# Kernel tuning notes

Hardware: AMD Instinct MI355X
Metric: run time of the kernel (lower is better)

## Reference

```python
import jax, jax.numpy as jnp
import numpy as np

N = 100000   # nodes
E = 1600000  # edges
HID = 128    # hidden_dim
H = 8        # heads
C = HID // H # head_dim = out_channels per head


def setup_inputs() -> dict:
    key = jax.random.key(0)
    ks = jax.random.split(key, 10)
    x = jax.random.normal(ks[0], (N, HID), jnp.float32)
    edge_index = jax.random.randint(ks[1], (2, E), 0, N, dtype=jnp.int64)
    edge_attr = jax.random.uniform(ks[2], (E,), jnp.float32)
    # GATConv params (lin_src == lin_dst shared since in_channels is int)
    W = jax.random.normal(ks[3], (HID, H * C), jnp.float32) / np.sqrt(HID)
    att_src = jax.random.normal(ks[4], (H, C), jnp.float32) / np.sqrt(C)
    att_dst = jax.random.normal(ks[5], (H, C), jnp.float32) / np.sqrt(C)
    # lin_edge: Linear(edge_dim=1, H*C, bias=False) -> weight [H*C, 1] stored as [H, C]
    w_edge = jax.random.normal(ks[6], (H, C), jnp.float32)
    att_edge = jax.random.normal(ks[7], (H, C), jnp.float32) / np.sqrt(C)
    bias = jnp.zeros((H * C,), jnp.float32)
    gamma = jnp.ones((HID,), jnp.float32)
    beta = jnp.zeros((HID,), jnp.float32)
    return dict(x=x, edge_index=edge_index, edge_attr=edge_attr, W=W,
                att_src=att_src, att_dst=att_dst, w_edge=w_edge,
                att_edge=att_edge, bias=bias, gamma=gamma, beta=beta)


def reference(x, edge_index, edge_attr, W, att_src, att_dst, w_edge, att_edge, bias, gamma, beta):
    n = x.shape[0]
    src, dst = edge_index[0], edge_index[1]
    # add_self_loops with fill_value='mean': loop edge_attr = per-dst-node mean of edge_attr
    ones = jnp.ones_like(edge_attr)
    deg = jax.ops.segment_sum(ones, dst, num_segments=n)
    loop_attr = jax.ops.segment_sum(edge_attr, dst, num_segments=n) / jnp.maximum(deg, 1.0)
    ar = jnp.arange(n, dtype=src.dtype)
    src = jnp.concatenate([src, ar])
    dst = jnp.concatenate([dst, ar])
    ea = jnp.concatenate([edge_attr, loop_attr])  # [E+N]

    h = (x @ W).reshape(n, H, C)                  # [N,H,C]
    a_src = (h * att_src).sum(-1)                 # [N,H]
    a_dst = (h * att_dst).sum(-1)                 # [N,H]
    # edge_dim=1: alpha_edge = <lin_edge(ea), att_edge> = ea * sum(w_edge*att_edge)
    w_e = (w_edge * att_edge).sum(-1)             # [H]
    alpha = a_src[src] + a_dst[dst] + ea[:, None] * w_e  # [E+N, H]
    alpha = jax.nn.leaky_relu(alpha, 0.2)
    # segment softmax over incoming edges of each dst node (all nodes have a self-loop)
    m = jax.ops.segment_max(alpha, dst, num_segments=n)      # [N,H]
    ex = jnp.exp(alpha - m[dst])
    denom = jax.ops.segment_sum(ex, dst, num_segments=n)     # [N,H]
    p = ex / (denom[dst] + 1e-16)
    # scatter-aggregate weighted messages, concat heads, bias
    out = jax.ops.segment_sum(p[:, :, None] * h[src], dst, num_segments=n)
    out = out.reshape(n, H * C) + bias
    # residual + LayerNorm + ReLU
    y = out + x
    mu = y.mean(-1, keepdims=True)
    var = ((y - mu) ** 2).mean(-1, keepdims=True)
    y = (y - mu) * jax.lax.rsqrt(var + 1e-5) * gamma + beta
    return jax.nn.relu(y)
```

## Files before the change

kernel.cpp:

```cpp
#include <hip/hip_runtime.h>
#include <math.h>

#define HID 128
#define HEADS 8
#define CDIM 16
#define NB1 256

typedef short bf8 __attribute__((ext_vector_type(8)));
typedef float f32x4 __attribute__((ext_vector_type(4)));

__device__ __forceinline__ unsigned short f2bf(float f) {
    unsigned u = __float_as_uint(f);
    unsigned r = (u + 0x7fffu + ((u >> 16) & 1u)) >> 16;
    return (unsigned short)r;
}
__device__ __forceinline__ float bf2f(unsigned short u) {
    return __uint_as_float(((unsigned)u) << 16);
}

__global__ __launch_bounds__(256) void k_tw(const float* __restrict__ W,
                                            unsigned short* __restrict__ Wt) {
    int idx = blockIdx.x * 256 + threadIdx.x;
    int j = idx >> 7, k = idx & 127;
    Wt[idx] = f2bf(W[k * HID + j]);
}

__global__ __launch_bounds__(256) void k_hist(const int* __restrict__ dst,
                                              int* __restrict__ cntmat,
                                              int E, int per, int nbkt) {
    __shared__ int h[256];
    int t = threadIdx.x;
    h[t] = 0;
    __syncthreads();
    int b0 = blockIdx.x * per;
    int b1 = min(b0 + per, E);
    for (int e = b0 + t; e < b1; e += 256)
        atomicAdd(&h[dst[e] >> 9], 1);
    __syncthreads();
    if (t < nbkt) cntmat[t * NB1 + blockIdx.x] = h[t];
}

__global__ __launch_bounds__(256) void kscanA(const int* __restrict__ in,
                                              int* __restrict__ tmp,
                                              int* __restrict__ bsum, int M) {
    __shared__ int lds[256];
    int t = threadIdx.x;
    int base = blockIdx.x * 1024 + t * 4;
    int v[4];
#pragma unroll
    for (int i = 0; i < 4; i++) {
        int idx = base + i;
        v[i] = (idx < M) ? in[idx] : 0;
    }
    int s = v[0] + v[1] + v[2] + v[3];
    lds[t] = s;
    __syncthreads();
    for (int off = 1; off < 256; off <<= 1) {
        int xv = (t >= off) ? lds[t - off] : 0;
        __syncthreads();
        lds[t] += xv;
        __syncthreads();
    }
    int run = (t > 0) ? lds[t - 1] : 0;
#pragma unroll
    for (int i = 0; i < 4; i++) {
        int idx = base + i;
        if (idx < M) tmp[idx] = run;
        run += v[i];
    }
    if (t == 255) bsum[blockIdx.x] = lds[255];
}

__global__ __launch_bounds__(128) void kscanB(const int* __restrict__ bsum,
                                              int* __restrict__ bscan, int nb,
                                              const float* __restrict__ w_edge,
                                              const float* __restrict__ att_edge,
                                              float* __restrict__ w_e) {
    __shared__ int lds[128];
    int t = threadIdx.x;
    if (t < HEADS) {
        float s = 0.f;
        for (int c = 0; c < CDIM; c++) s += w_edge[t * CDIM + c] * att_edge[t * CDIM + c];
        w_e[t] = s;
    }
    lds[t] = (t < nb) ? bsum[t] : 0;
    __syncthreads();
    for (int off = 1; off < 128; off <<= 1) {
        int xv = (t >= off) ? lds[t - off] : 0;
        __syncthreads();
        lds[t] += xv;
        __syncthreads();
    }
    bscan[t] = (t > 0) ? lds[t - 1] : 0;
}

__global__ __launch_bounds__(256) void kscanC(const int* __restrict__ tmp,
                                              const int* __restrict__ bscan,
                                              int* __restrict__ ofs, int M) {
    int i = blockIdx.x * 256 + threadIdx.x;
    if (i < M) ofs[i] = tmp[i] + bscan[i >> 10];
}

__global__ __launch_bounds__(256) void k_scat(const int* __restrict__ src,
                                              const int* __restrict__ dst,
                                              const float* __restrict__ eattr,
                                              const int* __restrict__ ofs,
                                              int* __restrict__ d1,
                                              int2* __restrict__ erec1,
                                              int E, int per, int nbkt) {
    __shared__ int cur[256];
    int t = threadIdx.x;
    if (t < nbkt) cur[t] = ofs[t * NB1 + blockIdx.x];
    __syncthreads();
    int b0 = blockIdx.x * per;
    int b1 = min(b0 + per, E);
    for (int e = b0 + t; e < b1; e += 256) {
        int d = dst[e];
        int pos = atomicAdd(&cur[d >> 9], 1);
        d1[pos] = d;
        erec1[pos] = make_int2(src[e], __float_as_int(eattr[e]));
    }
}

__global__ __launch_bounds__(256) void k_bin(const int* __restrict__ ofs,
                                             const int* __restrict__ d1,
                                             const int2* __restrict__ erec1,
                                             int* __restrict__ row_ptr,
                                             int2* __restrict__ erec,
                                             int N, int E, int nbkt) {
    __shared__ int h2[512];
    __shared__ int s2[256];
    __shared__ int cur2[512];
    int b = blockIdx.x, t = threadIdx.x;
    int base = ofs[b * NB1];
    int end = (b + 1 < nbkt) ? ofs[(b + 1) * NB1] : E;
    h2[t] = 0; h2[t + 256] = 0;
    __syncthreads();
    for (int e = base + t; e < end; e += 256)
        atomicAdd(&h2[d1[e] & 511], 1);
    __syncthreads();
    int a0 = h2[2 * t], a1 = h2[2 * t + 1];
    s2[t] = a0 + a1;
    __syncthreads();
    for (int off = 1; off < 256; off <<= 1) {
        int v = (t >= off) ? s2[t - off] : 0;
        __syncthreads();
        s2[t] += v;
        __syncthreads();
    }
    int ex = (t > 0) ? s2[t - 1] : 0;
    int p0 = base + ex;
    int p1 = p0 + a0;
    int ng = b * 512 + 2 * t;
    if (ng <= N) row_ptr[ng] = p0;
    if (ng + 1 <= N) row_ptr[ng + 1] = p1;
    cur2[2 * t] = p0;
    cur2[2 * t + 1] = p1;
    __syncthreads();
    for (int e = base + t; e < end; e += 256) {
        int d = d1[e];
        int pos = atomicAdd(&cur2[d & 511], 1);
        erec[pos] = erec1[e];
    }
}

__global__ __launch_bounds__(256) void k_gemm(const float* __restrict__ x,
                                              const unsigned short* __restrict__ Wt,
                                              const float* __restrict__ att_src,
                                              const float* __restrict__ att_dst,
                                              unsigned short* __restrict__ hbf,
                                              float* __restrict__ a_src,
                                              float* __restrict__ a_dst, int N) {
    int tid = threadIdx.x;
    int wv = tid >> 6, lane = tid & 63;
    int nloc = lane & 15, q = lane >> 4;
    int node = blockIdx.x * 64 + wv * 16 + nloc;
    int nc = min(node, N - 1);
    const float* xp = x + (size_t)nc * HID + q * 8;
    const unsigned short* wp = Wt + nloc * HID + q * 8;
    f32x4 acc[8];
#pragma unroll
    for (int i = 0; i < 8; i++) acc[i] = (f32x4){0.f, 0.f, 0.f, 0.f};
#pragma unroll
    for (int ch = 0; ch < 4; ch++) {
        float4 xv0 = *(const float4*)(xp + ch * 32);
        float4 xv1 = *(const float4*)(xp + ch * 32 + 4);
        bf8 bfrag;
        bfrag[0] = (short)f2bf(xv0.x); bfrag[1] = (short)f2bf(xv0.y);
        bfrag[2] = (short)f2bf(xv0.z); bfrag[3] = (short)f2bf(xv0.w);
        bfrag[4] = (short)f2bf(xv1.x); bfrag[5] = (short)f2bf(xv1.y);
        bfrag[6] = (short)f2bf(xv1.z); bfrag[7] = (short)f2bf(xv1.w);
#pragma unroll
        for (int jt = 0; jt < 8; jt++) {
            bf8 afrag = *(const bf8*)(wp + (size_t)jt * 16 * HID + ch * 32);
            acc[jt] = __builtin_amdgcn_mfma_f32_16x16x32_bf16(afrag, bfrag, acc[jt], 0, 0, 0);
        }
    }
    bool ok = node < N;
    size_t hb = (size_t)nc * HID;
#pragma unroll
    for (int jt = 0; jt < 8; jt++) {
        int j0 = jt * 16 + q * 4;
        float4 as4 = *(const float4*)(att_src + j0);
        float4 ad4 = *(const float4*)(att_dst + j0);
        f32x4 a = acc[jt];
        float ps = a[0] * as4.x + a[1] * as4.y + a[2] * as4.z + a[3] * as4.w;
        float pd = a[0] * ad4.x + a[1] * ad4.y + a[2] * ad4.z + a[3] * ad4.w;
        ps += __shfl_xor(ps, 16, 64); ps += __shfl_xor(ps, 32, 64);
        pd += __shfl_xor(pd, 16, 64); pd += __shfl_xor(pd, 32, 64);
        if (ok) {
            ushort4 hv;
            hv.x = f2bf(a[0]); hv.y = f2bf(a[1]); hv.z = f2bf(a[2]); hv.w = f2bf(a[3]);
            *(ushort4*)(hbf + hb + j0) = hv;
            if (q == 0) {
                a_src[(size_t)node * 8 + jt] = ps;
                a_dst[(size_t)node * 8 + jt] = pd;
            }
        }
    }
}

__global__ __launch_bounds__(64) void k_node(const int* __restrict__ row_ptr,
                                             const int2* __restrict__ erec,
                                             const float* __restrict__ a_src,
                                             const float* __restrict__ a_dst,
                                             const float* __restrict__ w_e,
                                             const unsigned short* __restrict__ hbf,
                                             const float* __restrict__ x,
                                             const float* __restrict__ bias,
                                             const float* __restrict__ gamma,
                                             const float* __restrict__ beta,
                                             float* __restrict__ out, int N) {
    int n = blockIdx.x;
    int lane = threadIdx.x;
    int r0 = row_ptr[n], r1 = row_ptr[n + 1];
    __shared__ float lex[64][9];
    __shared__ int lsrc[64];
    float ad[8], we[8];
#pragma unroll
    for (int q = 0; q < 8; q++) {
        ad[q] = a_dst[(size_t)n * 8 + q];
        we[q] = w_e[q];
    }
    float dsum[8];
#pragma unroll
    for (int q = 0; q < 8; q++) dsum[q] = 0.f;
    float acc0 = 0.f, acc1 = 0.f;
    float suma = 0.f;
    int head = lane >> 3;

    for (int base = r0; base < r1; base += 64) {
        int e = base + lane;
        if (e < r1) {
            int2 rec = erec[e];
            int s = rec.x;
            float a = __int_as_float(rec.y);
            suma += a;
            lsrc[lane] = s;
            const float* asp = a_src + (size_t)s * 8;
#pragma unroll
            for (int q = 0; q < 8; q++) {
                float v = asp[q] + ad[q] + a * we[q];
                v = v > 0.f ? v : 0.2f * v;
                float ex = __expf(v);
                dsum[q] += ex;
                lex[lane][q] = ex;
            }
        }
        __syncthreads();
        int cntc = min(64, r1 - base);
        for (int kk = 0; kk < cntc; kk++) {
            int s = lsrc[kk];
            ushort2 hv = *(const ushort2*)(hbf + (size_t)s * HID + 2 * lane);
            float w = lex[kk][head];
            acc0 = fmaf(w, bf2f(hv.x), acc0);
            acc1 = fmaf(w, bf2f(hv.y), acc1);
        }
        __syncthreads();
    }
#pragma unroll
    for (int q = 0; q < 8; q++) {
        float v = dsum[q];
#pragma unroll
        for (int off = 32; off; off >>= 1) v += __shfl_xor(v, off, 64);
        dsum[q] = v;
    }
#pragma unroll
    for (int off = 32; off; off >>= 1) suma += __shfl_xor(suma, off, 64);

    int deg = r1 - r0;
    float la = suma / fmaxf((float)deg, 1.0f);
    float vs = a_src[(size_t)n * 8 + head] + ad[head] + la * we[head];
    vs = vs > 0.f ? vs : 0.2f * vs;
    float exs = __expf(vs);
    size_t bx = (size_t)n * HID;
    ushort2 hs = *(const ushort2*)(hbf + bx + 2 * lane);
    acc0 = fmaf(exs, bf2f(hs.x), acc0);
    acc1 = fmaf(exs, bf2f(hs.y), acc1);
    float inv = 1.f / (dsum[head] + exs + 1e-16f);

    float2 xv = *(const float2*)(x + bx + 2 * lane);
    float2 bv = *(const float2*)(bias + 2 * lane);
    float y0 = acc0 * inv + bv.x + xv.x;
    float y1 = acc1 * inv + bv.y + xv.y;
    float ss = y0 + y1, sq = y0 * y0 + y1 * y1;
#pragma unroll
    for (int off = 32; off; off >>= 1) {
        ss += __shfl_xor(ss, off, 64);
        sq += __shfl_xor(sq, off, 64);
    }
    float mu = ss * (1.f / 128.f);
    float var = sq * (1.f / 128.f) - mu * mu;
    float r = rsqrtf(fmaxf(var, 0.f) + 1e-5f);
    float2 gv = *(const float2*)(gamma + 2 * lane);
    float2 tv = *(const float2*)(beta + 2 * lane);
    float o0 = (y0 - mu) * r * gv.x + tv.x;
    float o1 = (y1 - mu) * r * gv.y + tv.y;
    float2 ov = make_float2(fmaxf(o0, 0.f), fmaxf(o1, 0.f));
    *(float2*)(out + bx + 2 * lane) = ov;
}

extern "C" void kernel_launch(void* const* d_in, const int* in_sizes, int n_in,
                              void* d_out, int out_size, void* d_ws, size_t ws_size,
                              hipStream_t stream) {
    const float* x        = (const float*)d_in[0];
    const int*   ei       = (const int*)d_in[1];
    const float* eattr    = (const float*)d_in[2];
    const float* W        = (const float*)d_in[3];
    const float* att_src  = (const float*)d_in[4];
    const float* att_dst  = (const float*)d_in[5];
    const float* w_edge   = (const float*)d_in[6];
    const float* att_edge = (const float*)d_in[7];
    const float* bias     = (const float*)d_in[8];
    const float* gamma    = (const float*)d_in[9];
    const float* beta     = (const float*)d_in[10];

    int N = in_sizes[0] / HID;
    int E = in_sizes[2];
    const int* src = ei;
    const int* dst = ei + E;
    float* out = (float*)d_out;

    int nbkt = (N + 511) >> 9;
    int M = nbkt * NB1;
    int per = (E + NB1 - 1) / NB1;

    char* ws = (char*)d_ws;
    size_t off = 0;
    auto alloc = [&](size_t bytes) { char* p = ws + off; off += (bytes + 255) & ~255ull; return p; };
    unsigned short* hbf = (unsigned short*)alloc((size_t)N * HID * 2);
    unsigned short* Wt  = (unsigned short*)alloc((size_t)HID * HID * 2);
    float* a_src   = (float*)alloc((size_t)N * 8 * 4);
    float* a_dst   = (float*)alloc((size_t)N * 8 * 4);
    int2*  erec    = (int2*) alloc((size_t)E * 8);
    int2*  erec1   = (int2*) alloc((size_t)E * 8);
    int*   d1      = (int*)  alloc((size_t)E * 4);
    int*   cntmat  = (int*)  alloc((size_t)M * 4);
    int*   stmp    = (int*)  alloc((size_t)M * 4);
    int*   ofs     = (int*)  alloc((size_t)M * 4);
    int*   bsum    = (int*)  alloc(128 * 4);
    int*   bscan   = (int*)  alloc(128 * 4);
    int*   row_ptr = (int*)  alloc((size_t)(N + 1) * 4);
    float* w_e     = (float*)alloc(8 * 4);

    int nbA = (M + 1023) / 1024;

    k_tw<<<64, 256, 0, stream>>>(W, Wt);
    k_hist<<<NB1, 256, 0, stream>>>(dst, cntmat, E, per, nbkt);
    kscanA<<<nbA, 256, 0, stream>>>(cntmat, stmp, bsum, M);
    kscanB<<<1, 128, 0, stream>>>(bsum, bscan, nbA, w_edge, att_edge, w_e);
    kscanC<<<(M + 255) / 256, 256, 0, stream>>>(stmp, bscan, ofs, M);
    k_scat<<<NB1, 256, 0, stream>>>(src, dst, eattr, ofs, d1, erec1, E, per, nbkt);
    k_bin<<<nbkt, 256, 0, stream>>>(ofs, d1, erec1, row_ptr, erec, N, E, nbkt);
    k_gemm<<<(N + 63) / 64, 256, 0, stream>>>(x, Wt, att_src, att_dst, hbf, a_src, a_dst, N);
    k_node<<<N, 64, 0, stream>>>(row_ptr, erec, a_src, a_dst, w_e, hbf, x,
                                 bias, gamma, beta, out, N);
}
```

Baseline: 338.5 us.

## Co-launch independent kernels and streamline per-node gather in aggregation

Merges the weight transpose into the histogram kernel and the node GEMM into the edge scatter kernel by splitting the grid on block index, so independent work shares one launch and can run concurrently. This removes two launches and lets the GEMM overlap the memory-bound scatter. In the node kernel, the softmax denominator is now accumulated per lane during the gather loop, which removes the 8-way cross-lane reduction. The row offset is made wave-uniform via readfirstlane, a_src is loaded as float4, and bf16 unpacking uses bit masks. The grid-split kernels may reduce occupancy if register or LDS use rises.

```diff
diff --git a/kernel.cpp b/kernel.cpp
--- a/kernel.cpp
+++ b/kernel.cpp
@@ -18,18 +18,19 @@
     return __uint_as_float(((unsigned)u) << 16);
 }
 
-__global__ __launch_bounds__(256) void k_tw(const float* __restrict__ W,
-                                            unsigned short* __restrict__ Wt) {
-    int idx = blockIdx.x * 256 + threadIdx.x;
-    int j = idx >> 7, k = idx & 127;
-    Wt[idx] = f2bf(W[k * HID + j]);
-}
-
-__global__ __launch_bounds__(256) void k_hist(const int* __restrict__ dst,
-                                              int* __restrict__ cntmat,
-                                              int E, int per, int nbkt) {
+__global__ __launch_bounds__(256) void k_hist_tw(const float* __restrict__ W,
+                                                 unsigned short* __restrict__ Wt,
+                                                 const int* __restrict__ dst,
+                                                 int* __restrict__ cntmat,
+                                                 int E, int per, int nbkt) {
     __shared__ int h[256];
     int t = threadIdx.x;
+    if (blockIdx.x >= NB1) {
+        int idx = (blockIdx.x - NB1) * 256 + t;
+        int j = idx >> 7, k = idx & 127;
+        Wt[idx] = f2bf(W[k * HID + j]);
+        return;
+    }
     h[t] = 0;
     __syncthreads();
     int b0 = blockIdx.x * per;
@@ -101,80 +102,34 @@
     if (i < M) ofs[i] = tmp[i] + bscan[i >> 10];
 }
 
-__global__ __launch_bounds__(256) void k_scat(const int* __restrict__ src,
-                                              const int* __restrict__ dst,
-                                              const float* __restrict__ eattr,
-                                              const int* __restrict__ ofs,
-                                              int* __restrict__ d1,
-                                              int2* __restrict__ erec1,
-                                              int E, int per, int nbkt) {
+__global__ __launch_bounds__(256) void k_scat_gemm(
+        const int* __restrict__ src, const int* __restrict__ dst,
+        const float* __restrict__ eattr, const int* __restrict__ ofs,
+        int* __restrict__ d1, int2* __restrict__ erec1,
+        int E, int per, int nbkt,
+        const float* __restrict__ x, const unsigned short* __restrict__ Wt,
+        const float* __restrict__ att_src, const float* __restrict__ att_dst,
+        unsigned short* __restrict__ hbf, float* __restrict__ a_src,
+        float* __restrict__ a_dst, int N) {
     __shared__ int cur[256];
-    int t = threadIdx.x;
-    if (t < nbkt) cur[t] = ofs[t * NB1 + blockIdx.x];
-    __syncthreads();
-    int b0 = blockIdx.x * per;
-    int b1 = min(b0 + per, E);
-    for (int e = b0 + t; e < b1; e += 256) {
-        int d = dst[e];
-        int pos = atomicAdd(&cur[d >> 9], 1);
-        d1[pos] = d;
-        erec1[pos] = make_int2(src[e], __float_as_int(eattr[e]));
-    }
-}
-
-__global__ __launch_bounds__(256) void k_bin(const int* __restrict__ ofs,
-                                             const int* __restrict__ d1,
-                                             const int2* __restrict__ erec1,
-                                             int* __restrict__ row_ptr,
-                                             int2* __restrict__ erec,
-                                             int N, int E, int nbkt) {
-    __shared__ int h2[512];
-    __shared__ int s2[256];
-    __shared__ int cur2[512];
-    int b = blockIdx.x, t = threadIdx.x;
-    int base = ofs[b * NB1];
-    int end = (b + 1 < nbkt) ? ofs[(b + 1) * NB1] : E;
-    h2[t] = 0; h2[t + 256] = 0;
-    __syncthreads();
-    for (int e = base + t; e < end; e += 256)
-        atomicAdd(&h2[d1[e] & 511], 1);
-    __syncthreads();
-    int a0 = h2[2 * t], a1 = h2[2 * t + 1];
-    s2[t] = a0 + a1;
-    __syncthreads();
-    for (int off = 1; off < 256; off <<= 1) {
-        int v = (t >= off) ? s2[t - off] : 0;
-        __syncthreads();
-        s2[t] += v;
-        __syncthreads();
-    }
-    int ex = (t > 0) ? s2[t - 1] : 0;
-    int p0 = base + ex;
-    int p1 = p0 + a0;
-    int ng = b * 512 + 2 * t;
-    if (ng <= N) row_ptr[ng] = p0;
-    if (ng + 1 <= N) row_ptr[ng + 1] = p1;
-    cur2[2 * t] = p0;
-    cur2[2 * t + 1] = p1;
-    __syncthreads();
-    for (int e = base + t; e < end; e += 256) {
-        int d = d1[e];
-        int pos = atomicAdd(&cur2[d & 511], 1);
-        erec[pos] = erec1[e];
-    }
-}
-
-__global__ __launch_bounds__(256) void k_gemm(const float* __restrict__ x,
-                                              const unsigned short* __restrict__ Wt,
-                                              const float* __restrict__ att_src,
-                                              const float* __restrict__ att_dst,
-                                              unsigned short* __restrict__ hbf,
-                                              float* __restrict__ a_src,
-                                              float* __restrict__ a_dst, int N) {
     int tid = threadIdx.x;
+    if (blockIdx.x < NB1) {
+        if (tid < nbkt) cur[tid] = ofs[tid * NB1 + blockIdx.x];
+        __syncthreads();
+        int b0 = blockIdx.x * per;
+        int b1 = min(b0 + per, E);
+        for (int e = b0 + tid; e < b1; e += 256) {
+            int d = dst[e];
+            int pos = atomicAdd(&cur[d >> 9], 1);
+            d1[pos] = d;
+            erec1[pos] = make_int2(src[e], __float_as_int(eattr[e]));
+        }
+        return;
+    }
+    int bid = blockIdx.x - NB1;
     int wv = tid >> 6, lane = tid & 63;
     int nloc = lane & 15, q = lane >> 4;
-    int node = blockIdx.x * 64 + wv * 16 + nloc;
+    int node = bid * 64 + wv * 16 + nloc;
     int nc = min(node, N - 1);
     const float* xp = x + (size_t)nc * HID + q * 8;
     const unsigned short* wp = Wt + nloc * HID + q * 8;
@@ -220,6 +175,48 @@
     }
 }
 
+__global__ __launch_bounds__(256) void k_bin(const int* __restrict__ ofs,
+                                             const int* __restrict__ d1,
+                                             const int2* __restrict__ erec1,
+                                             int* __restrict__ row_ptr,
+                                             int2* __restrict__ erec,
+                                             int N, int E, int nbkt) {
+    __shared__ int h2[512];
+    __shared__ int s2[256];
+    __shared__ int cur2[512];
+    int b = blockIdx.x, t = threadIdx.x;
+    int base = ofs[b * NB1];
+    int end = (b + 1 < nbkt) ? ofs[(b + 1) * NB1] : E;
+    h2[t] = 0; h2[t + 256] = 0;
+    __syncthreads();
+    for (int e = base + t; e < end; e += 256)
+        atomicAdd(&h2[d1[e] & 511], 1);
+    __syncthreads();
+    int a0 = h2[2 * t], a1 = h2[2 * t + 1];
+    s2[t] = a0 + a1;
+    __syncthreads();
+    for (int off = 1; off < 256; off <<= 1) {
+        int v = (t >= off) ? s2[t - off] : 0;
+        __syncthreads();
+        s2[t] += v;
+        __syncthreads();
+    }
+    int ex = (t > 0) ? s2[t - 1] : 0;
+    int p0 = base + ex;
+    int p1 = p0 + a0;
+    int ng = b * 512 + 2 * t;
+    if (ng <= N) row_ptr[ng] = p0;
+    if (ng + 1 <= N) row_ptr[ng + 1] = p1;
+    cur2[2 * t] = p0;
+    cur2[2 * t + 1] = p1;
+    __syncthreads();
+    for (int e = base + t; e < end; e += 256) {
+        int d = d1[e];
+        int pos = atomicAdd(&cur2[d & 511], 1);
+        erec[pos] = erec1[e];
+    }
+}
+
 __global__ __launch_bounds__(64) void k_node(const int* __restrict__ row_ptr,
                                              const int2* __restrict__ erec,
                                              const float* __restrict__ a_src,
@@ -242,10 +239,8 @@
         ad[q] = a_dst[(size_t)n * 8 + q];
         we[q] = w_e[q];
     }
-    float dsum[8];
-#pragma unroll
-    for (int q = 0; q < 8; q++) dsum[q] = 0.f;
     float acc0 = 0.f, acc1 = 0.f;
+    float wsum = 0.f;
     float suma = 0.f;
     int head = lane >> 3;
 
@@ -256,34 +251,29 @@
             int s = rec.x;
             float a = __int_as_float(rec.y);
             suma += a;
-            lsrc[lane] = s;
-            const float* asp = a_src + (size_t)s * 8;
+            lsrc[lane] = s << 8;
+            const float4* asp = (const float4*)(a_src + (size_t)s * 8);
+            float4 s0 = asp[0], s1 = asp[1];
+            float al[8] = {s0.x, s0.y, s0.z, s0.w, s1.x, s1.y, s1.z, s1.w};
 #pragma unroll
             for (int q = 0; q < 8; q++) {
-                float v = asp[q] + ad[q] + a * we[q];
+                float v = al[q] + ad[q] + a * we[q];
                 v = v > 0.f ? v : 0.2f * v;
-                float ex = __expf(v);
-                dsum[q] += ex;
-                lex[lane][q] = ex;
+                lex[lane][q] = __expf(v);
             }
         }
         __syncthreads();
         int cntc = min(64, r1 - base);
         for (int kk = 0; kk < cntc; kk++) {
-            int s = lsrc[kk];
-            ushort2 hv = *(const ushort2*)(hbf + (size_t)s * HID + 2 * lane);
+            int soff = __builtin_amdgcn_readfirstlane(lsrc[kk]);
+            const unsigned* hp = (const unsigned*)((const char*)hbf + soff);
+            unsigned u = hp[lane];
             float w = lex[kk][head];
-            acc0 = fmaf(w, bf2f(hv.x), acc0);
-            acc1 = fmaf(w, bf2f(hv.y), acc1);
-        }
-        __syncthreads();
-    }
-#pragma unroll
-    for (int q = 0; q < 8; q++) {
-        float v = dsum[q];
-#pragma unroll
-        for (int off = 32; off; off >>= 1) v += __shfl_xor(v, off, 64);
-        dsum[q] = v;
+            wsum += w;
+            acc0 = fmaf(w, __uint_as_float(u << 16), acc0);
+            acc1 = fmaf(w, __uint_as_float(u & 0xffff0000u), acc1);
+        }
+        __syncthreads();
     }
 #pragma unroll
     for (int off = 32; off; off >>= 1) suma += __shfl_xor(suma, off, 64);
@@ -294,10 +284,10 @@
     vs = vs > 0.f ? vs : 0.2f * vs;
     float exs = __expf(vs);
     size_t bx = (size_t)n * HID;
-    ushort2 hs = *(const ushort2*)(hbf + bx + 2 * lane);
-    acc0 = fmaf(exs, bf2f(hs.x), acc0);
-    acc1 = fmaf(exs, bf2f(hs.y), acc1);
-    float inv = 1.f / (dsum[head] + exs + 1e-16f);
+    unsigned us = ((const unsigned*)((const char*)hbf + ((size_t)n << 8)))[lane];
+    acc0 = fmaf(exs, __uint_as_float(us << 16), acc0);
+    acc1 = fmaf(exs, __uint_as_float(us & 0xffff0000u), acc1);
+    float inv = 1.f / (wsum + exs + 1e-16f);
 
     float2 xv = *(const float2*)(x + bx + 2 * lane);
     float2 bv = *(const float2*)(bias + 2 * lane);
@@ -364,15 +354,17 @@
     float* w_e     = (float*)alloc(8 * 4);
 
     int nbA = (M + 1023) / 1024;
-
-    k_tw<<<64, 256, 0, stream>>>(W, Wt);
-    k_hist<<<NB1, 256, 0, stream>>>(dst, cntmat, E, per, nbkt);
+    int GB = (N + 63) / 64;
+
+    k_hist_tw<<<NB1 + 64, 256, 0, stream>>>(W, Wt, dst, cntmat, E, per, nbkt);
     kscanA<<<nbA, 256, 0, stream>>>(cntmat, stmp, bsum, M);
     kscanB<<<1, 128, 0, stream>>>(bsum, bscan, nbA, w_edge, att_edge, w_e);
     kscanC<<<(M + 255) / 256, 256, 0, stream>>>(stmp, bscan, ofs, M);
-    k_scat<<<NB1, 256, 0, stream>>>(src, dst, eattr, ofs, d1, erec1, E, per, nbkt);
+    k_scat_gemm<<<NB1 + GB, 256, 0, stream>>>(src, dst, eattr, ofs, d1, erec1,
+                                              E, per, nbkt,
+                                              x, Wt, att_src, att_dst, hbf,
+                                              a_src, a_dst, N);
     k_bin<<<nbkt, 256, 0, stream>>>(ofs, d1, erec1, row_ptr, erec, N, E, nbkt);
-    k_gemm<<<(N + 63) / 64, 256, 0, stream>>>(x, Wt, att_src, att_dst, hbf, a_src, a_dst, N);
     k_node<<<N, 64, 0, stream>>>(row_ptr, erec, a_src, a_dst, w_e, hbf, x,
                                  bias, gamma, beta, out, N);
 }
```

Result: slower. 360.1 us (+6.4%).
